# Optimization experiments

Hardware: AMD Instinct MI355X
Metric: run time of the kernel (lower is better)

The kernel has to match this reference:

```python
import jax, jax.numpy as jnp
import numpy as np

B, T, d, D = 256, 1024, 4, 32  # batch, seqlen, physical dim, bond dim


def setup_inputs() -> dict:
    key = jax.random.key(0)
    k1, k2, k3, k4 = jax.random.split(key, 4)
    X = jax.random.randint(k1, (B, T), 0, d)  # categorical sequences
    k_core = (d * D * D) ** -0.5
    k_vec = d ** -0.5
    # 'noisy' init: ones + 0.5*gaussian, scaled as in __init__
    core = (k_core * (1.0 + 0.5 * jax.random.normal(k2, (d, D, D)))).astype(jnp.float32)
    left_boundary = (k_vec * (1.0 + 0.5 * jax.random.normal(k3, (D,)))).astype(jnp.float32)
    right_boundary = (k_vec * (1.0 + 0.5 * jax.random.normal(k4, (D,)))).astype(jnp.float32)
    return {"X": X, "core": core, "left_boundary": left_boundary,
            "right_boundary": right_boundary}


def reference(X, core, left_boundary, right_boundary):
    """Batched _log_contract_at: log P(x) per sequence via sequential TT
    contraction with infinity-norm rescaling at every step.
    Returns logprobs of shape [B]."""
    batch = X.shape[0]
    Z0 = jnp.max(jnp.abs(left_boundary))  # vec_norm (inf norm)
    v0 = jnp.broadcast_to(left_boundary / Z0, (batch, D))
    acc0 = jnp.full((batch,), jnp.log(Z0), dtype=left_boundary.dtype)

    def step(carry, x_t):
        v, acc = carry
        M = core[x_t]                              # [B, D, D] gathered cores
        v2 = jnp.einsum('bi,bij->bj', v, M)        # running contraction
        Z = jnp.max(jnp.abs(v2), axis=1)           # per-seq inf norm
        return (v2 / Z[:, None], acc + jnp.log(Z)), None

    (v, acc), _ = jax.lax.scan(step, (v0, acc0), X.T)  # scan over seqlen
    out = jnp.einsum('bi,i->b', v, right_boundary)
    # original: log((exp(acc)*out).abs()**2) == 2*(acc + log|out|)
    logprobs = 2.0 * (acc + jnp.log(jnp.abs(out)))
    return logprobs
```

## Files before the change

kernel.cpp:

```cpp
#include <hip/hip_runtime.h>
#include <math.h>


#define TT_B 256
#define TT_T 1024

typedef __attribute__((ext_vector_type(8))) short bf16x8;
typedef __attribute__((ext_vector_type(4))) float f32x4;

__device__ uint4 g_QT[256 * 2 * 64];
__device__ int   g_kQ[256];

__device__ __forceinline__ unsigned pkbf16(float lo, float hi)
{
    unsigned r;
    asm volatile("v_cvt_pk_bf16_f32 %0, %1, %2" : "=v"(r) : "v"(lo), "v"(hi));
    return r;
}
__device__ __forceinline__ bf16x8 as_bf16x8(int4 v)
{ union { int4 i; bf16x8 h; } u; u.i = v; return u.h; }
__device__ __forceinline__ bf16x8 as_bf16x8u(uint4 v)
{ union { uint4 i; bf16x8 h; } u; u.i = v; return u.h; }


__device__ __forceinline__ void mm32(const float* __restrict__ AT,
                                     const float* __restrict__ B,
                                     int h, int j, float c[16])
{
#pragma unroll
    for (int r = 0; r < 16; ++r) c[r] = 0.f;
#pragma unroll 4
    for (int k = 0; k < 32; ++k) {
        float bv = B[k * 32 + j];
        const float4* ar = (const float4*)(AT + k * 36 + 16 * h);
        float4 a0 = ar[0], a1 = ar[1], a2 = ar[2], a3 = ar[3];
        c[ 0] = fmaf(a0.x, bv, c[ 0]); c[ 1] = fmaf(a0.y, bv, c[ 1]);
        c[ 2] = fmaf(a0.z, bv, c[ 2]); c[ 3] = fmaf(a0.w, bv, c[ 3]);
        c[ 4] = fmaf(a1.x, bv, c[ 4]); c[ 5] = fmaf(a1.y, bv, c[ 5]);
        c[ 6] = fmaf(a1.z, bv, c[ 6]); c[ 7] = fmaf(a1.w, bv, c[ 7]);
        c[ 8] = fmaf(a2.x, bv, c[ 8]); c[ 9] = fmaf(a2.y, bv, c[ 9]);
        c[10] = fmaf(a2.z, bv, c[10]); c[11] = fmaf(a2.w, bv, c[11]);
        c[12] = fmaf(a3.x, bv, c[12]); c[13] = fmaf(a3.y, bv, c[13]);
        c[14] = fmaf(a3.z, bv, c[14]); c[15] = fmaf(a3.w, bv, c[15]);
    }
}

__device__ __forceinline__ void load_transpose(const float* __restrict__ src,
                                               float* __restrict__ dstT, int lane)
{
    const float4* s4 = (const float4*)src;
    float4 v0 = s4[lane * 4 + 0], v1 = s4[lane * 4 + 1];
    float4 v2 = s4[lane * 4 + 2], v3 = s4[lane * 4 + 3];
    const int ro = lane >> 1;
    const int k0 = (lane & 1) * 16;
    dstT[(k0 +  0) * 36 + ro] = v0.x; dstT[(k0 +  1) * 36 + ro] = v0.y;
    dstT[(k0 +  2) * 36 + ro] = v0.z; dstT[(k0 +  3) * 36 + ro] = v0.w;
    dstT[(k0 +  4) * 36 + ro] = v1.x; dstT[(k0 +  5) * 36 + ro] = v1.y;
    dstT[(k0 +  6) * 36 + ro] = v1.z; dstT[(k0 +  7) * 36 + ro] = v1.w;
    dstT[(k0 +  8) * 36 + ro] = v2.x; dstT[(k0 +  9) * 36 + ro] = v2.y;
    dstT[(k0 + 10) * 36 + ro] = v2.z; dstT[(k0 + 11) * 36 + ro] = v2.w;
    dstT[(k0 + 12) * 36 + ro] = v3.x; dstT[(k0 + 13) * 36 + ro] = v3.y;
    dstT[(k0 + 14) * 36 + ro] = v3.z; dstT[(k0 + 15) * 36 + ro] = v3.w;
}

__device__ __forceinline__ void load_straight(const float* __restrict__ src,
                                              float* __restrict__ dst, int lane)
{
    const float4* s4 = (const float4*)src;
    float4* d4 = (float4*)dst;
    d4[lane * 4 + 0] = s4[lane * 4 + 0];
    d4[lane * 4 + 1] = s4[lane * 4 + 1];
    d4[lane * 4 + 2] = s4[lane * 4 + 2];
    d4[lane * 4 + 3] = s4[lane * 4 + 3];
}

__global__ __launch_bounds__(64) void tt_quad_kernel(const float* __restrict__ core)
{
    __shared__ float AT [32 * 36];
    __shared__ float Bb [32 * 32];
    __shared__ float A2T[32 * 36];
    __shared__ float B2 [32 * 32];
    __shared__ float Qs [32 * 33];

    const int m    = blockIdx.x;
    const int lane = threadIdx.x;
    const int h    = lane >> 5;
    const int j    = lane & 31;

    const int ia = (m >> 6) & 3;
    const int ib = (m >> 4) & 3;
    const int ic = (m >> 2) & 3;
    const int id =  m       & 3;

    float c[16];

    load_transpose(core + ia * 1024, AT, lane);
    load_straight (core + ib * 1024, Bb, lane);
    __syncthreads();
    mm32(AT, Bb, h, j, c);
    __syncthreads();
    {
        float4* dst = (float4*)(A2T + j * 36 + 16 * h);
        dst[0] = make_float4(c[ 0], c[ 1], c[ 2], c[ 3]);
        dst[1] = make_float4(c[ 4], c[ 5], c[ 6], c[ 7]);
        dst[2] = make_float4(c[ 8], c[ 9], c[10], c[11]);
        dst[3] = make_float4(c[12], c[13], c[14], c[15]);
    }
    __syncthreads();

    load_transpose(core + ic * 1024, AT, lane);
    load_straight (core + id * 1024, Bb, lane);
    __syncthreads();
    mm32(AT, Bb, h, j, c);
    __syncthreads();
#pragma unroll
    for (int r = 0; r < 16; ++r) B2[(16 * h + r) * 32 + j] = c[r];
    __syncthreads();

    mm32(A2T, B2, h, j, c);

    float ssum = 0.f;
#pragma unroll
    for (int r = 0; r < 16; ++r) ssum += fabsf(c[r]);
    ssum += __shfl_xor(ssum, 32);
    float cm = ssum;
    cm = fmaxf(cm, __shfl_xor(cm,  1));
    cm = fmaxf(cm, __shfl_xor(cm,  2));
    cm = fmaxf(cm, __shfl_xor(cm,  4));
    cm = fmaxf(cm, __shfl_xor(cm,  8));
    cm = fmaxf(cm, __shfl_xor(cm, 16));
    const int eb = __float_as_int(cm) & 0x7f800000;
    const float s = __int_as_float(0x7F000000 - eb);
#pragma unroll
    for (int r = 0; r < 16; ++r) c[r] *= s;
    if (lane == 0) g_kQ[m] = (eb >> 23) - 127;

#pragma unroll
    for (int r = 0; r < 16; ++r) Qs[(16 * h + r) * 33 + j] = c[r];
    __syncthreads();

    const int g  = lane >> 4;
    const int jj = lane & 15;
#pragma unroll
    for (int H = 0; H < 2; ++H) {
        const int cb = 16 * H + jj;
        uint4 wf;
        wf.x = pkbf16(Qs[(4*g+0)*33 + cb],  Qs[(4*g+1)*33 + cb]);
        wf.y = pkbf16(Qs[(4*g+2)*33 + cb],  Qs[(4*g+3)*33 + cb]);
        wf.z = pkbf16(Qs[(16+4*g+0)*33 + cb], Qs[(16+4*g+1)*33 + cb]);
        wf.w = pkbf16(Qs[(16+4*g+2)*33 + cb], Qs[(16+4*g+3)*33 + cb]);
        g_QT[(m * 2 + H) * 64 + lane] = wf;
    }
}


#define MAXD4(D) fmaxf(fmaxf(fabsf(D[0]), fabsf(D[1])), fmaxf(fabsf(D[2]), fabsf(D[3])))

#define LOAD2(UB0, UB1, MIDX) do {                                            \
    const int voff_ = (((MIDX) << 11) | (lane << 4));                         \
    asm volatile("global_load_dwordx4 %0, %1, %2"             : "=v"(UB0) : "v"(voff_), "s"(qtb)); \
    asm volatile("global_load_dwordx4 %0, %1, %2 offset:1024" : "=v"(UB1) : "v"(voff_), "s"(qtb)); \
} while (0)

#define MSTEP(UB0, UB1, MIDX, DO_SCALE, DO_MEAS, DO_LAST) do {                \
    const bf16x8 sb0 = as_bf16x8u(make_uint4(S0w, S1w, S2w, S3w));            \
    const bf16x8 sb1 = as_bf16x8u(make_uint4(S4w, S5w, S6w, S7w));            \
    asm volatile("s_waitcnt vmcnt(6)" ::: "memory");                          \
    __builtin_amdgcn_sched_barrier(0);                                        \
    const bf16x8 af0 = as_bf16x8(UB0);                                        \
    const bf16x8 af1 = as_bf16x8(UB1);                                        \
    f32x4 d00 = __builtin_amdgcn_mfma_f32_16x16x32_bf16(af0, sb0, zero, 0, 0, 0); \
    f32x4 d01 = __builtin_amdgcn_mfma_f32_16x16x32_bf16(af0, sb1, zero, 0, 0, 0); \
    f32x4 d10 = __builtin_amdgcn_mfma_f32_16x16x32_bf16(af1, sb0, zero, 0, 0, 0); \
    f32x4 d11 = __builtin_amdgcn_mfma_f32_16x16x32_bf16(af1, sb1, zero, 0, 0, 0); \
    LOAD2(UB0, UB1, (MIDX));                                                  \
    if (DO_SCALE) {                                                           \
        _Pragma("unroll") for (int r_ = 0; r_ < 4; ++r_) {                    \
            d00[r_] *= s_apply; d01[r_] *= s_apply;                           \
            d10[r_] *= s_apply; d11[r_] *= s_apply;                           \
        }                                                                     \
        Ecorr += 127 - ((__float_as_int(s_apply) >> 23) & 0xFF);              \
    }                                                                         \
    if (DO_MEAS) {                                                            \
        zmeas = fmaxf(fmaxf(MAXD4(d00), MAXD4(d01)),                          \
                      fmaxf(MAXD4(d10), MAXD4(d11)));                         \
    }                                                                         \
    if (DO_LAST) {                                                            \
        _Pragma("unroll") for (int u_ = 0; u_ < 4; ++u_) {                    \
            Mseg[(4*g + u_) * 36 + jj]           = d00[u_];                   \
            Mseg[(4*g + u_) * 36 + 16 + jj]      = d01[u_];                   \
            Mseg[(16 + 4*g + u_) * 36 + jj]      = d10[u_];                   \
            Mseg[(16 + 4*g + u_) * 36 + 16 + jj] = d11[u_];                   \
        }                                                                     \
    } else {                                                                  \
        S0w = pkbf16(d00[0], d00[1]);  S1w = pkbf16(d00[2], d00[3]);          \
        S2w = pkbf16(d10[0], d10[1]);  S3w = pkbf16(d10[2], d10[3]);          \
        S4w = pkbf16(d01[0], d01[1]);  S5w = pkbf16(d01[2], d01[3]);          \
        S6w = pkbf16(d11[0], d11[1]);  S7w = pkbf16(d11[2], d11[3]);          \
    }                                                                         \
} while (0)

__device__ __forceinline__ int tree_node_lds(const float* __restrict__ Ma,
                                             const float* __restrict__ Mb,
                                             float* __restrict__ Mdst, int lane)
{
    const int p = lane & 15, q = lane >> 4;
    const float4 a00 = *(const float4*)(Mb + p * 36 + 8 * q);
    const float4 a01 = *(const float4*)(Mb + p * 36 + 8 * q + 4);
    const float4 a10 = *(const float4*)(Mb + (16 + p) * 36 + 8 * q);
    const float4 a11 = *(const float4*)(Mb + (16 + p) * 36 + 8 * q + 4);
    int4 aw0, aw1;
    aw0.x = (int)pkbf16(a00.x, a00.y); aw0.y = (int)pkbf16(a00.z, a00.w);
    aw0.z = (int)pkbf16(a01.x, a01.y); aw0.w = (int)pkbf16(a01.z, a01.w);
    aw1.x = (int)pkbf16(a10.x, a10.y); aw1.y = (int)pkbf16(a10.z, a10.w);
    aw1.z = (int)pkbf16(a11.x, a11.y); aw1.w = (int)pkbf16(a11.z, a11.w);
    int4 bw0, bw1;
    bw0.x = (int)pkbf16(Ma[(8*q+0)*36 + p], Ma[(8*q+1)*36 + p]);
    bw0.y = (int)pkbf16(Ma[(8*q+2)*36 + p], Ma[(8*q+3)*36 + p]);
    bw0.z = (int)pkbf16(Ma[(8*q+4)*36 + p], Ma[(8*q+5)*36 + p]);
    bw0.w = (int)pkbf16(Ma[(8*q+6)*36 + p], Ma[(8*q+7)*36 + p]);
    bw1.x = (int)pkbf16(Ma[(8*q+0)*36 + 16 + p], Ma[(8*q+1)*36 + 16 + p]);
    bw1.y = (int)pkbf16(Ma[(8*q+2)*36 + 16 + p], Ma[(8*q+3)*36 + 16 + p]);
    bw1.z = (int)pkbf16(Ma[(8*q+4)*36 + 16 + p], Ma[(8*q+5)*36 + 16 + p]);
    bw1.w = (int)pkbf16(Ma[(8*q+6)*36 + 16 + p], Ma[(8*q+7)*36 + 16 + p]);

    const bf16x8 af0 = as_bf16x8(aw0), af1 = as_bf16x8(aw1);
    const bf16x8 bf0 = as_bf16x8(bw0), bf1 = as_bf16x8(bw1);
    const f32x4 zero = {0.f, 0.f, 0.f, 0.f};
    f32x4 d00 = __builtin_amdgcn_mfma_f32_16x16x32_bf16(af0, bf0, zero, 0, 0, 0);
    f32x4 d01 = __builtin_amdgcn_mfma_f32_16x16x32_bf16(af0, bf1, zero, 0, 0, 0);
    f32x4 d10 = __builtin_amdgcn_mfma_f32_16x16x32_bf16(af1, bf0, zero, 0, 0, 0);
    f32x4 d11 = __builtin_amdgcn_mfma_f32_16x16x32_bf16(af1, bf1, zero, 0, 0, 0);

    float zm = fmaxf(fmaxf(MAXD4(d00), MAXD4(d01)), fmaxf(MAXD4(d10), MAXD4(d11)));
    zm = fmaxf(zm, __shfl_xor(zm,  1));
    zm = fmaxf(zm, __shfl_xor(zm,  2));
    zm = fmaxf(zm, __shfl_xor(zm,  4));
    zm = fmaxf(zm, __shfl_xor(zm,  8));
    zm = fmaxf(zm, __shfl_xor(zm, 16));
    zm = fmaxf(zm, __shfl_xor(zm, 32));
    const int eb = __float_as_int(zm) & 0x7f800000;
    const float s = __int_as_float(0x7F000000 - eb);
#pragma unroll
    for (int t = 0; t < 4; ++t) {
        Mdst[(4*q + t) * 36 + p]           = d00[t] * s;
        Mdst[(4*q + t) * 36 + 16 + p]      = d01[t] * s;
        Mdst[(16 + 4*q + t) * 36 + p]      = d10[t] * s;
        Mdst[(16 + 4*q + t) * 36 + 16 + p] = d11[t] * s;
    }
    return (eb >> 23) - 127;
}

__global__ __launch_bounds__(512, 1) void tt_main_kernel(const int* __restrict__ X,
                                                         const float* __restrict__ Lb,
                                                         const float* __restrict__ Rb,
                                                         float* __restrict__ out)
{
    __shared__ int   idxs[272];
    __shared__ __align__(16) float Ms[15 * 1152];
    __shared__ int   EcA[16];
    __shared__ int   kpart[8];

    const int b    = blockIdx.x;
    const int tid  = threadIdx.x;
    const int wid  = tid >> 6;
    const int lane = tid & 63;

    int ksum = 0;
    if (tid < 256) {
        const int4 xv = ((const int4*)(X + (size_t)b * TT_T))[tid];
        const int m = ((xv.x * 4 + xv.y) * 4 + xv.z) * 4 + xv.w;
        idxs[tid] = m;
        ksum = g_kQ[m];
    }
    if (tid >= 256 && tid < 272) idxs[tid] = 0;
    if (tid < 16) EcA[tid] = 0;
    ksum += __shfl_xor(ksum,  1);
    ksum += __shfl_xor(ksum,  2);
    ksum += __shfl_xor(ksum,  4);
    ksum += __shfl_xor(ksum,  8);
    ksum += __shfl_xor(ksum, 16);
    ksum += __shfl_xor(ksum, 32);
    if (lane == 0) kpart[wid] = ksum;
    __syncthreads();

    const uint4* qtb = g_QT;
    const f32x4 zero = {0.f, 0.f, 0.f, 0.f};

    const int base4 = 8 * wid;
    const int4* idxs4 = (const int4*)idxs;
    const int g = lane >> 4, jj = lane & 15;
    float* Mseg = Ms + wid * 1152;

    unsigned S0w, S1w, S2w, S3w, S4w, S5w, S6w, S7w;
    {
        const unsigned e0 = ((4*g+0 == jj) ? 0x3F80u : 0u) | ((4*g+1 == jj) ? 0x3F800000u : 0u);
        const unsigned e1 = ((4*g+2 == jj) ? 0x3F80u : 0u) | ((4*g+3 == jj) ? 0x3F800000u : 0u);
        S0w = e0; S1w = e1; S2w = 0u; S3w = 0u;
        S4w = 0u; S5w = 0u; S6w = e0; S7w = e1;
    }

    int   Ecorr = 0;
    float s_apply = 1.0f, zmeas = 1.0f;

    int4 Ba0, Ba1, Bb0, Bb1, Bc0, Bc1, Bd0, Bd1;
    {
        const int4 m0 = idxs4[base4];
        LOAD2(Ba0, Ba1, m0.x);
        LOAD2(Bb0, Bb1, m0.y);
        LOAD2(Bc0, Bc1, m0.z);
        LOAD2(Bd0, Bd1, m0.w);
    }
    int4 mqc = idxs4[base4 + 1];

#pragma unroll 1
    for (int J = 0; J < 8; ++J) {
        const int4 mq_nx = idxs4[base4 + J + 2];

        const bool sc = (J == 2 || J == 4 || J == 6);
        const bool ms = (J == 1 || J == 3 || J == 5);
        const bool lt = (J == 7);

        MSTEP(Ba0, Ba1, mqc.x, sc, 0, 0);
        MSTEP(Bb0, Bb1, mqc.y, 0, 0, 0);
        MSTEP(Bc0, Bc1, mqc.z, 0, 0, 0);
        MSTEP(Bd0, Bd1, mqc.w, 0, ms, lt);

        if (ms) {
            float z = zmeas;
            z = fmaxf(z, __shfl_xor(z,  1));
            z = fmaxf(z, __shfl_xor(z,  2));
            z = fmaxf(z, __shfl_xor(z,  4));
            z = fmaxf(z, __shfl_xor(z,  8));
            z = fmaxf(z, __shfl_xor(z, 16));
            z = fmaxf(z, __shfl_xor(z, 32));
            const int eb = __float_as_int(z) & 0x7f800000;
            s_apply = __int_as_float(0x7F000000 - eb);
        }
        mqc = mq_nx;
    }

    asm volatile("s_waitcnt vmcnt(0)" ::: "memory");

    if (lane == 0) EcA[wid] = Ecorr;
    __syncthreads();

    if (wid < 4) {
        const int ec = tree_node_lds(Ms + (2*wid) * 1152, Ms + (2*wid + 1) * 1152,
                                     Ms + (8 + wid) * 1152, lane);
        if (lane == 0) EcA[8 + wid] = ec;
    }
    __syncthreads();
    if (wid < 2) {
        const int ec = tree_node_lds(Ms + (8 + 2*wid) * 1152, Ms + (8 + 2*wid + 1) * 1152,
                                     Ms + (12 + wid) * 1152, lane);
        if (lane == 0) EcA[12 + wid] = ec;
    }
    __syncthreads();
    int ecL3 = 0;
    if (wid == 0) {
        ecL3 = tree_node_lds(Ms + 12 * 1152, Ms + 13 * 1152, Ms + 14 * 1152, lane);
    }
    __syncthreads();

    if (wid == 0 && lane < 32) {
        const float* Mt = Ms + 14 * 1152;
        float v = 0.f;
#pragma unroll 8
        for (int c2 = 0; c2 < 32; ++c2) v = fmaf(Rb[c2], Mt[c2 * 36 + lane], v);
        float p = v * Lb[lane];
        p += __shfl_xor(p,  1);
        p += __shfl_xor(p,  2);
        p += __shfl_xor(p,  4);
        p += __shfl_xor(p,  8);
        p += __shfl_xor(p, 16);
        if (lane == 0) {
            int S = ecL3;
#pragma unroll
            for (int w = 0; w < 16; ++w) S += EcA[w];
#pragma unroll
            for (int w = 0; w < 8; ++w) S += kpart[w];
            out[b] = 2.0f * ((float)S * 0.6931471805599453f + logf(fabsf(p)));
        }
    }
}

extern "C" void kernel_launch(void* const* d_in, const int* in_sizes, int n_in,
                              void* d_out, int out_size, void* d_ws, size_t ws_size,
                              hipStream_t stream)
{
    const int*   X    = (const int*)d_in[0];
    const float* core = (const float*)d_in[1];
    const float* Lb   = (const float*)d_in[2];
    const float* Rb   = (const float*)d_in[3];
    float* out = (float*)d_out;

    tt_quad_kernel<<<dim3(256), dim3(64), 0, stream>>>(core);
    tt_main_kernel<<<dim3(256), dim3(512), 0, stream>>>(X, Lb, Rb, out);
}
```

Baseline: 21.98 us.

## Double main-kernel waves to 16, shorten chains, add tree level, drop mid-chain rescale

The main kernel now runs 1024 threads (16 waves), so each wave's serial MFMA chain covers 16 quad-matrices instead of 32, and one more level is added to the LDS reduction tree. Because the chains are shorter, the periodic max-measure and rescale inside the chain loop are removed. The quad-precompute kernel also swaps its scalar fp32 mm32 products for tree_node_lds calls and folds their exponents into g_kQ. The aim is to halve the serial dependency latency per block. The cost is an extra tree level with barriers and more LDS, and dropping the rescale relies on 16 unscaled bf16 products staying in range.

```diff
diff --git a/kernel.cpp b/kernel.cpp
--- a/kernel.cpp
+++ b/kernel.cpp
@@ -22,183 +22,7 @@
 __device__ __forceinline__ bf16x8 as_bf16x8u(uint4 v)
 { union { uint4 i; bf16x8 h; } u; u.i = v; return u.h; }
 
-
-__device__ __forceinline__ void mm32(const float* __restrict__ AT,
-                                     const float* __restrict__ B,
-                                     int h, int j, float c[16])
-{
-#pragma unroll
-    for (int r = 0; r < 16; ++r) c[r] = 0.f;
-#pragma unroll 4
-    for (int k = 0; k < 32; ++k) {
-        float bv = B[k * 32 + j];
-        const float4* ar = (const float4*)(AT + k * 36 + 16 * h);
-        float4 a0 = ar[0], a1 = ar[1], a2 = ar[2], a3 = ar[3];
-        c[ 0] = fmaf(a0.x, bv, c[ 0]); c[ 1] = fmaf(a0.y, bv, c[ 1]);
-        c[ 2] = fmaf(a0.z, bv, c[ 2]); c[ 3] = fmaf(a0.w, bv, c[ 3]);
-        c[ 4] = fmaf(a1.x, bv, c[ 4]); c[ 5] = fmaf(a1.y, bv, c[ 5]);
-        c[ 6] = fmaf(a1.z, bv, c[ 6]); c[ 7] = fmaf(a1.w, bv, c[ 7]);
-        c[ 8] = fmaf(a2.x, bv, c[ 8]); c[ 9] = fmaf(a2.y, bv, c[ 9]);
-        c[10] = fmaf(a2.z, bv, c[10]); c[11] = fmaf(a2.w, bv, c[11]);
-        c[12] = fmaf(a3.x, bv, c[12]); c[13] = fmaf(a3.y, bv, c[13]);
-        c[14] = fmaf(a3.z, bv, c[14]); c[15] = fmaf(a3.w, bv, c[15]);
-    }
-}
-
-__device__ __forceinline__ void load_transpose(const float* __restrict__ src,
-                                               float* __restrict__ dstT, int lane)
-{
-    const float4* s4 = (const float4*)src;
-    float4 v0 = s4[lane * 4 + 0], v1 = s4[lane * 4 + 1];
-    float4 v2 = s4[lane * 4 + 2], v3 = s4[lane * 4 + 3];
-    const int ro = lane >> 1;
-    const int k0 = (lane & 1) * 16;
-    dstT[(k0 +  0) * 36 + ro] = v0.x; dstT[(k0 +  1) * 36 + ro] = v0.y;
-    dstT[(k0 +  2) * 36 + ro] = v0.z; dstT[(k0 +  3) * 36 + ro] = v0.w;
-    dstT[(k0 +  4) * 36 + ro] = v1.x; dstT[(k0 +  5) * 36 + ro] = v1.y;
-    dstT[(k0 +  6) * 36 + ro] = v1.z; dstT[(k0 +  7) * 36 + ro] = v1.w;
-    dstT[(k0 +  8) * 36 + ro] = v2.x; dstT[(k0 +  9) * 36 + ro] = v2.y;
-    dstT[(k0 + 10) * 36 + ro] = v2.z; dstT[(k0 + 11) * 36 + ro] = v2.w;
-    dstT[(k0 + 12) * 36 + ro] = v3.x; dstT[(k0 + 13) * 36 + ro] = v3.y;
-    dstT[(k0 + 14) * 36 + ro] = v3.z; dstT[(k0 + 15) * 36 + ro] = v3.w;
-}
-
-__device__ __forceinline__ void load_straight(const float* __restrict__ src,
-                                              float* __restrict__ dst, int lane)
-{
-    const float4* s4 = (const float4*)src;
-    float4* d4 = (float4*)dst;
-    d4[lane * 4 + 0] = s4[lane * 4 + 0];
-    d4[lane * 4 + 1] = s4[lane * 4 + 1];
-    d4[lane * 4 + 2] = s4[lane * 4 + 2];
-    d4[lane * 4 + 3] = s4[lane * 4 + 3];
-}
-
-__global__ __launch_bounds__(64) void tt_quad_kernel(const float* __restrict__ core)
-{
-    __shared__ float AT [32 * 36];
-    __shared__ float Bb [32 * 32];
-    __shared__ float A2T[32 * 36];
-    __shared__ float B2 [32 * 32];
-    __shared__ float Qs [32 * 33];
-
-    const int m    = blockIdx.x;
-    const int lane = threadIdx.x;
-    const int h    = lane >> 5;
-    const int j    = lane & 31;
-
-    const int ia = (m >> 6) & 3;
-    const int ib = (m >> 4) & 3;
-    const int ic = (m >> 2) & 3;
-    const int id =  m       & 3;
-
-    float c[16];
-
-    load_transpose(core + ia * 1024, AT, lane);
-    load_straight (core + ib * 1024, Bb, lane);
-    __syncthreads();
-    mm32(AT, Bb, h, j, c);
-    __syncthreads();
-    {
-        float4* dst = (float4*)(A2T + j * 36 + 16 * h);
-        dst[0] = make_float4(c[ 0], c[ 1], c[ 2], c[ 3]);
-        dst[1] = make_float4(c[ 4], c[ 5], c[ 6], c[ 7]);
-        dst[2] = make_float4(c[ 8], c[ 9], c[10], c[11]);
-        dst[3] = make_float4(c[12], c[13], c[14], c[15]);
-    }
-    __syncthreads();
-
-    load_transpose(core + ic * 1024, AT, lane);
-    load_straight (core + id * 1024, Bb, lane);
-    __syncthreads();
-    mm32(AT, Bb, h, j, c);
-    __syncthreads();
-#pragma unroll
-    for (int r = 0; r < 16; ++r) B2[(16 * h + r) * 32 + j] = c[r];
-    __syncthreads();
-
-    mm32(A2T, B2, h, j, c);
-
-    float ssum = 0.f;
-#pragma unroll
-    for (int r = 0; r < 16; ++r) ssum += fabsf(c[r]);
-    ssum += __shfl_xor(ssum, 32);
-    float cm = ssum;
-    cm = fmaxf(cm, __shfl_xor(cm,  1));
-    cm = fmaxf(cm, __shfl_xor(cm,  2));
-    cm = fmaxf(cm, __shfl_xor(cm,  4));
-    cm = fmaxf(cm, __shfl_xor(cm,  8));
-    cm = fmaxf(cm, __shfl_xor(cm, 16));
-    const int eb = __float_as_int(cm) & 0x7f800000;
-    const float s = __int_as_float(0x7F000000 - eb);
-#pragma unroll
-    for (int r = 0; r < 16; ++r) c[r] *= s;
-    if (lane == 0) g_kQ[m] = (eb >> 23) - 127;
-
-#pragma unroll
-    for (int r = 0; r < 16; ++r) Qs[(16 * h + r) * 33 + j] = c[r];
-    __syncthreads();
-
-    const int g  = lane >> 4;
-    const int jj = lane & 15;
-#pragma unroll
-    for (int H = 0; H < 2; ++H) {
-        const int cb = 16 * H + jj;
-        uint4 wf;
-        wf.x = pkbf16(Qs[(4*g+0)*33 + cb],  Qs[(4*g+1)*33 + cb]);
-        wf.y = pkbf16(Qs[(4*g+2)*33 + cb],  Qs[(4*g+3)*33 + cb]);
-        wf.z = pkbf16(Qs[(16+4*g+0)*33 + cb], Qs[(16+4*g+1)*33 + cb]);
-        wf.w = pkbf16(Qs[(16+4*g+2)*33 + cb], Qs[(16+4*g+3)*33 + cb]);
-        g_QT[(m * 2 + H) * 64 + lane] = wf;
-    }
-}
-
-
 #define MAXD4(D) fmaxf(fmaxf(fabsf(D[0]), fabsf(D[1])), fmaxf(fabsf(D[2]), fabsf(D[3])))
-
-#define LOAD2(UB0, UB1, MIDX) do {                                            \
-    const int voff_ = (((MIDX) << 11) | (lane << 4));                         \
-    asm volatile("global_load_dwordx4 %0, %1, %2"             : "=v"(UB0) : "v"(voff_), "s"(qtb)); \
-    asm volatile("global_load_dwordx4 %0, %1, %2 offset:1024" : "=v"(UB1) : "v"(voff_), "s"(qtb)); \
-} while (0)
-
-#define MSTEP(UB0, UB1, MIDX, DO_SCALE, DO_MEAS, DO_LAST) do {                \
-    const bf16x8 sb0 = as_bf16x8u(make_uint4(S0w, S1w, S2w, S3w));            \
-    const bf16x8 sb1 = as_bf16x8u(make_uint4(S4w, S5w, S6w, S7w));            \
-    asm volatile("s_waitcnt vmcnt(6)" ::: "memory");                          \
-    __builtin_amdgcn_sched_barrier(0);                                        \
-    const bf16x8 af0 = as_bf16x8(UB0);                                        \
-    const bf16x8 af1 = as_bf16x8(UB1);                                        \
-    f32x4 d00 = __builtin_amdgcn_mfma_f32_16x16x32_bf16(af0, sb0, zero, 0, 0, 0); \
-    f32x4 d01 = __builtin_amdgcn_mfma_f32_16x16x32_bf16(af0, sb1, zero, 0, 0, 0); \
-    f32x4 d10 = __builtin_amdgcn_mfma_f32_16x16x32_bf16(af1, sb0, zero, 0, 0, 0); \
-    f32x4 d11 = __builtin_amdgcn_mfma_f32_16x16x32_bf16(af1, sb1, zero, 0, 0, 0); \
-    LOAD2(UB0, UB1, (MIDX));                                                  \
-    if (DO_SCALE) {                                                           \
-        _Pragma("unroll") for (int r_ = 0; r_ < 4; ++r_) {                    \
-            d00[r_] *= s_apply; d01[r_] *= s_apply;                           \
-            d10[r_] *= s_apply; d11[r_] *= s_apply;                           \
-        }                                                                     \
-        Ecorr += 127 - ((__float_as_int(s_apply) >> 23) & 0xFF);              \
-    }                                                                         \
-    if (DO_MEAS) {                                                            \
-        zmeas = fmaxf(fmaxf(MAXD4(d00), MAXD4(d01)),                          \
-                      fmaxf(MAXD4(d10), MAXD4(d11)));                         \
-    }                                                                         \
-    if (DO_LAST) {                                                            \
-        _Pragma("unroll") for (int u_ = 0; u_ < 4; ++u_) {                    \
-            Mseg[(4*g + u_) * 36 + jj]           = d00[u_];                   \
-            Mseg[(4*g + u_) * 36 + 16 + jj]      = d01[u_];                   \
-            Mseg[(16 + 4*g + u_) * 36 + jj]      = d10[u_];                   \
-            Mseg[(16 + 4*g + u_) * 36 + 16 + jj] = d11[u_];                   \
-        }                                                                     \
-    } else {                                                                  \
-        S0w = pkbf16(d00[0], d00[1]);  S1w = pkbf16(d00[2], d00[3]);          \
-        S2w = pkbf16(d10[0], d10[1]);  S3w = pkbf16(d10[2], d10[3]);          \
-        S4w = pkbf16(d01[0], d01[1]);  S5w = pkbf16(d01[2], d01[3]);          \
-        S6w = pkbf16(d11[0], d11[1]);  S7w = pkbf16(d11[2], d11[3]);          \
-    }                                                                         \
-} while (0)
 
 __device__ __forceinline__ int tree_node_lds(const float* __restrict__ Ma,
                                              const float* __restrict__ Mb,
@@ -251,15 +75,110 @@
     return (eb >> 23) - 127;
 }
 
-__global__ __launch_bounds__(512, 1) void tt_main_kernel(const int* __restrict__ X,
-                                                         const float* __restrict__ Lb,
-                                                         const float* __restrict__ Rb,
-                                                         float* __restrict__ out)
-{
-    __shared__ int   idxs[272];
-    __shared__ __align__(16) float Ms[15 * 1152];
+
+__global__ __launch_bounds__(64) void tt_quad_kernel(const float* __restrict__ core)
+{
+    __shared__ __align__(16) float Qb[6 * 1152];
+
+    const int m    = blockIdx.x;
+    const int lane = threadIdx.x;
+
+    const int ia = (m >> 6) & 3;
+    const int ib = (m >> 4) & 3;
+    const int ic = (m >> 2) & 3;
+    const int id =  m       & 3;
+
+    const int r  = lane >> 1;
+    const int hh = (lane & 1) * 16;
+#define LOADM(SLOT, IDX) do {                                                 \
+        const float4* s4_ = (const float4*)(core + (IDX) * 1024 + r * 32 + hh); \
+        float4 v0_ = s4_[0], v1_ = s4_[1], v2_ = s4_[2], v3_ = s4_[3];        \
+        float4* d4_ = (float4*)(Qb + (SLOT) * 1152 + r * 36 + hh);            \
+        d4_[0] = v0_; d4_[1] = v1_; d4_[2] = v2_; d4_[3] = v3_;               \
+    } while (0)
+    LOADM(0, ia); LOADM(1, ib); LOADM(2, ic); LOADM(3, id);
+#undef LOADM
+    __syncthreads();
+
+    const int e1 = tree_node_lds(Qb + 1 * 1152, Qb + 0 * 1152, Qb + 4 * 1152, lane);
+    const int e2 = tree_node_lds(Qb + 3 * 1152, Qb + 2 * 1152, Qb + 5 * 1152, lane);
+    __syncthreads();
+    const int e3 = tree_node_lds(Qb + 5 * 1152, Qb + 4 * 1152, Qb + 0 * 1152, lane);
+    __syncthreads();
+
+    const float* Qf = Qb;
+    const int h = lane >> 5, j = lane & 31;
+    float ssum = 0.f;
+#pragma unroll
+    for (int rr = 0; rr < 16; ++rr) ssum += fabsf(Qf[(16 * h + rr) * 36 + j]);
+    ssum += __shfl_xor(ssum, 32);
+    float cm = ssum;
+    cm = fmaxf(cm, __shfl_xor(cm,  1));
+    cm = fmaxf(cm, __shfl_xor(cm,  2));
+    cm = fmaxf(cm, __shfl_xor(cm,  4));
+    cm = fmaxf(cm, __shfl_xor(cm,  8));
+    cm = fmaxf(cm, __shfl_xor(cm, 16));
+    const int eb = __float_as_int(cm) & 0x7f800000;
+    const float s = __int_as_float(0x7F000000 - eb);
+    if (lane == 0) g_kQ[m] = ((eb >> 23) - 127) + e1 + e2 + e3;
+
+    const int g  = lane >> 4;
+    const int jj = lane & 15;
+#pragma unroll
+    for (int H = 0; H < 2; ++H) {
+        const int cb = 16 * H + jj;
+        uint4 wf;
+        wf.x = pkbf16(s * Qf[(4*g+0)*36 + cb],    s * Qf[(4*g+1)*36 + cb]);
+        wf.y = pkbf16(s * Qf[(4*g+2)*36 + cb],    s * Qf[(4*g+3)*36 + cb]);
+        wf.z = pkbf16(s * Qf[(16+4*g+0)*36 + cb], s * Qf[(16+4*g+1)*36 + cb]);
+        wf.w = pkbf16(s * Qf[(16+4*g+2)*36 + cb], s * Qf[(16+4*g+3)*36 + cb]);
+        g_QT[(m * 2 + H) * 64 + lane] = wf;
+    }
+}
+
+
+#define LOAD2(UB0, UB1, MIDX) do {                                            \
+    const int voff_ = (((MIDX) << 11) | (lane << 4));                         \
+    asm volatile("global_load_dwordx4 %0, %1, %2"             : "=v"(UB0) : "v"(voff_), "s"(qtb)); \
+    asm volatile("global_load_dwordx4 %0, %1, %2 offset:1024" : "=v"(UB1) : "v"(voff_), "s"(qtb)); \
+} while (0)
+
+#define MSTEP(UB0, UB1, MIDX, DO_LAST) do {                                   \
+    const bf16x8 sb0 = as_bf16x8u(make_uint4(S0w, S1w, S2w, S3w));            \
+    const bf16x8 sb1 = as_bf16x8u(make_uint4(S4w, S5w, S6w, S7w));            \
+    asm volatile("s_waitcnt vmcnt(6)" ::: "memory");                          \
+    __builtin_amdgcn_sched_barrier(0);                                        \
+    const bf16x8 af0 = as_bf16x8(UB0);                                        \
+    const bf16x8 af1 = as_bf16x8(UB1);                                        \
+    f32x4 d00 = __builtin_amdgcn_mfma_f32_16x16x32_bf16(af0, sb0, zero, 0, 0, 0); \
+    f32x4 d01 = __builtin_amdgcn_mfma_f32_16x16x32_bf16(af0, sb1, zero, 0, 0, 0); \
+    f32x4 d10 = __builtin_amdgcn_mfma_f32_16x16x32_bf16(af1, sb0, zero, 0, 0, 0); \
+    f32x4 d11 = __builtin_amdgcn_mfma_f32_16x16x32_bf16(af1, sb1, zero, 0, 0, 0); \
+    LOAD2(UB0, UB1, (MIDX));                                                  \
+    if (DO_LAST) {                                                            \
+        _Pragma("unroll") for (int u_ = 0; u_ < 4; ++u_) {                    \
+            Mseg[(4*g + u_) * 36 + jj]           = d00[u_];                   \
+            Mseg[(4*g + u_) * 36 + 16 + jj]      = d01[u_];                   \
+            Mseg[(16 + 4*g + u_) * 36 + jj]      = d10[u_];                   \
+            Mseg[(16 + 4*g + u_) * 36 + 16 + jj] = d11[u_];                   \
+        }                                                                     \
+    } else {                                                                  \
+        S0w = pkbf16(d00[0], d00[1]);  S1w = pkbf16(d00[2], d00[3]);          \
+        S2w = pkbf16(d10[0], d10[1]);  S3w = pkbf16(d10[2], d10[3]);          \
+        S4w = pkbf16(d01[0], d01[1]);  S5w = pkbf16(d01[2], d01[3]);          \
+        S6w = pkbf16(d11[0], d11[1]);  S7w = pkbf16(d11[2], d11[3]);          \
+    }                                                                         \
+} while (0)
+
+__global__ __launch_bounds__(1024, 1) void tt_main_kernel(const int* __restrict__ X,
+                                                          const float* __restrict__ Lb,
+                                                          const float* __restrict__ Rb,
+                                                          float* __restrict__ out)
+{
+    __shared__ __align__(16) int   idxs[272];
+    __shared__ __align__(16) float Ms[24 * 1152];
     __shared__ int   EcA[16];
-    __shared__ int   kpart[8];
+    __shared__ int   kpart[16];
 
     const int b    = blockIdx.x;
     const int tid  = threadIdx.x;
@@ -287,7 +206,7 @@
     const uint4* qtb = g_QT;
     const f32x4 zero = {0.f, 0.f, 0.f, 0.f};
 
-    const int base4 = 8 * wid;
+    const int base4 = 4 * wid;
     const int4* idxs4 = (const int4*)idxs;
     const int g = lane >> 4, jj = lane & 15;
     float* Mseg = Ms + wid * 1152;
@@ -299,9 +218,6 @@
         S0w = e0; S1w = e1; S2w = 0u; S3w = 0u;
         S4w = 0u; S5w = 0u; S6w = e0; S7w = e1;
     }
-
-    int   Ecorr = 0;
-    float s_apply = 1.0f, zmeas = 1.0f;
 
     int4 Ba0, Ba1, Bb0, Bb1, Bc0, Bc1, Bd0, Bd1;
     {
@@ -314,57 +230,45 @@
     int4 mqc = idxs4[base4 + 1];
 
 #pragma unroll 1
-    for (int J = 0; J < 8; ++J) {
+    for (int J = 0; J < 4; ++J) {
         const int4 mq_nx = idxs4[base4 + J + 2];
 
-        const bool sc = (J == 2 || J == 4 || J == 6);
-        const bool ms = (J == 1 || J == 3 || J == 5);
-        const bool lt = (J == 7);
-
-        MSTEP(Ba0, Ba1, mqc.x, sc, 0, 0);
-        MSTEP(Bb0, Bb1, mqc.y, 0, 0, 0);
-        MSTEP(Bc0, Bc1, mqc.z, 0, 0, 0);
-        MSTEP(Bd0, Bd1, mqc.w, 0, ms, lt);
-
-        if (ms) {
-            float z = zmeas;
-            z = fmaxf(z, __shfl_xor(z,  1));
-            z = fmaxf(z, __shfl_xor(z,  2));
-            z = fmaxf(z, __shfl_xor(z,  4));
-            z = fmaxf(z, __shfl_xor(z,  8));
-            z = fmaxf(z, __shfl_xor(z, 16));
-            z = fmaxf(z, __shfl_xor(z, 32));
-            const int eb = __float_as_int(z) & 0x7f800000;
-            s_apply = __int_as_float(0x7F000000 - eb);
-        }
+        const bool lt = (J == 3);
+        MSTEP(Ba0, Ba1, mqc.x, 0);
+        MSTEP(Bb0, Bb1, mqc.y, 0);
+        MSTEP(Bc0, Bc1, mqc.z, 0);
+        MSTEP(Bd0, Bd1, mqc.w, lt);
         mqc = mq_nx;
     }
 
     asm volatile("s_waitcnt vmcnt(0)" ::: "memory");
-
-    if (lane == 0) EcA[wid] = Ecorr;
-    __syncthreads();
-
+    __syncthreads();
+
+    if (wid < 8) {
+        const int ec = tree_node_lds(Ms + (2*wid) * 1152, Ms + (2*wid + 1) * 1152,
+                                     Ms + (16 + wid) * 1152, lane);
+        if (lane == 0) EcA[wid] = ec;
+    }
+    __syncthreads();
     if (wid < 4) {
+        const int ec = tree_node_lds(Ms + (16 + 2*wid) * 1152, Ms + (16 + 2*wid + 1) * 1152,
+                                     Ms + wid * 1152, lane);
+        if (lane == 0) EcA[8 + wid] = ec;
+    }
+    __syncthreads();
+    if (wid < 2) {
         const int ec = tree_node_lds(Ms + (2*wid) * 1152, Ms + (2*wid + 1) * 1152,
-                                     Ms + (8 + wid) * 1152, lane);
-        if (lane == 0) EcA[8 + wid] = ec;
-    }
-    __syncthreads();
-    if (wid < 2) {
-        const int ec = tree_node_lds(Ms + (8 + 2*wid) * 1152, Ms + (8 + 2*wid + 1) * 1152,
-                                     Ms + (12 + wid) * 1152, lane);
+                                     Ms + (16 + wid) * 1152, lane);
         if (lane == 0) EcA[12 + wid] = ec;
     }
     __syncthreads();
-    int ecL3 = 0;
+    int ecL4 = 0;
     if (wid == 0) {
-        ecL3 = tree_node_lds(Ms + 12 * 1152, Ms + 13 * 1152, Ms + 14 * 1152, lane);
-    }
-    __syncthreads();
+        ecL4 = tree_node_lds(Ms + 16 * 1152, Ms + 17 * 1152, Ms, lane);
+    }
 
     if (wid == 0 && lane < 32) {
-        const float* Mt = Ms + 14 * 1152;
+        const float* Mt = Ms;
         float v = 0.f;
 #pragma unroll 8
         for (int c2 = 0; c2 < 32; ++c2) v = fmaf(Rb[c2], Mt[c2 * 36 + lane], v);
@@ -375,11 +279,9 @@
         p += __shfl_xor(p,  8);
         p += __shfl_xor(p, 16);
         if (lane == 0) {
-            int S = ecL3;
+            int S = ecL4;
 #pragma unroll
-            for (int w = 0; w < 16; ++w) S += EcA[w];
-#pragma unroll
-            for (int w = 0; w < 8; ++w) S += kpart[w];
+            for (int w = 0; w < 16; ++w) S += EcA[w] + kpart[w];
             out[b] = 2.0f * ((float)S * 0.6931471805599453f + logf(fabsf(p)));
         }
     }
@@ -396,5 +298,5 @@
     float* out = (float*)d_out;
 
     tt_quad_kernel<<<dim3(256), dim3(64), 0, stream>>>(core);
-    tt_main_kernel<<<dim3(256), dim3(512), 0, stream>>>(X, Lb, Rb, out);
-}
+    tt_main_kernel<<<dim3(256), dim3(1024), 0, stream>>>(X, Lb, Rb, out);
+}
```

Measured after the change: 21.45 us. 2.4% less time.
